# Performance work log

Hardware: AMD Instinct MI355X
Metric: run time of the kernel (lower is better)

Reference implementation:

```python
import jax, jax.numpy as jnp
import numpy as np

COMMITMENT_COST = 0.25
EPS = 1e-12  # matches torch F.normalize default eps


def _l2norm(v, axis=-1):
    n = jnp.linalg.norm(v, axis=axis, keepdims=True)
    return v / jnp.maximum(n, EPS)


def setup_inputs() -> dict:
    key = jax.random.key(0)
    k1, k2 = jax.random.split(key)
    x = jax.random.normal(k1, (65536, 256), dtype=jnp.float32)
    codebook = jax.random.normal(k2, (4096, 256), dtype=jnp.float32)
    return {"x": x, "codebook": codebook}


def reference(x, codebook):
    # x: [N, D] latents; codebook: [K, D] embedding table
    xn = _l2norm(x)                 # [N, D]
    cbn = _l2norm(codebook)         # [K, D]

    # Squared L2 distances: ||xn||^2 + ||cbn||^2 - 2 xn.cbn^T  -> [N, K]
    dists = (
        jnp.sum(xn * xn, axis=-1, keepdims=True)
        + jnp.sum(cbn * cbn, axis=1)
        - 2.0 * jnp.einsum("nd,kd->nk", xn, cbn)
    )
    idx = jnp.argmin(dists, axis=1)  # [N]

    # quantize: gather then L2-normalize (matches F.normalize(embeddings(idx)))
    quantized = _l2norm(cbn[idx])    # [N, D]

    q_latent_loss = jnp.mean((quantized - jax.lax.stop_gradient(xn)) ** 2)
    e_latent_loss = jnp.mean((xn - jax.lax.stop_gradient(quantized)) ** 2)
    loss = q_latent_loss + COMMITMENT_COST * e_latent_loss

    # straight-through estimator
    quantized_st = xn + jax.lax.stop_gradient(quantized - xn)
    return quantized_st, loss, idx
```

## Files before the change

kernel.cpp:

```cpp
#include <hip/hip_runtime.h>
#include <math.h>

#define N_ROWS 65536
#define DIM    256
#define NCODE  4096
#define MARGIN 2e-4f
#define TILE_C 32
#define NTILE  (NCODE / TILE_C)
#define FB     8
#define KCH    1024
#define NCH    (NCODE / KCH)
#define FIXG   512

typedef __attribute__((ext_vector_type(8)))  short short8v;
typedef __attribute__((ext_vector_type(4)))  float float4v;
typedef __attribute__((ext_vector_type(16))) float f32x16;

__device__ inline unsigned short f2bf(float f) {
    unsigned u = __float_as_uint(f);
    unsigned r = (u + 0x7fffu + ((u >> 16) & 1u)) >> 16;
    return (unsigned short)r;
}
__device__ inline float bf2f(unsigned short h) {
    return __uint_as_float(((unsigned)h) << 16);
}
__device__ inline void gll16(const void* g, void* l) {
    __builtin_amdgcn_global_load_lds(
        (const __attribute__((address_space(1))) unsigned int*)g,
        (__attribute__((address_space(3))) unsigned int*)l, 16, 0, 0);
}

__global__ void cb_norm_kernel(const float* __restrict__ cb,
                               unsigned short* __restrict__ pk,
                               float* __restrict__ c2,
                               double* __restrict__ c2d,
                               double* __restrict__ ndi) {
    int k = blockIdx.x;
    int t = threadIdx.x;
    float v = cb[k * DIM + t];
    double dv = (double)v;
    double ss = dv * dv;
    __shared__ double red2[4], red3[4], redn[4];
    #pragma unroll
    for (int off = 32; off > 0; off >>= 1) ss += __shfl_down(ss, off);
    if ((t & 63) == 0) redn[t >> 6] = ss;
    __syncthreads();
    double S = redn[0] + redn[1] + redn[2] + redn[3];
    double nrm = fmax(sqrt(S), 1e-12);
    double cq = dv / nrm;
    float cf = (float)cq;
    unsigned short hb = f2bf(cf);
    unsigned short lb = f2bf(cf - bf2f(hb));
    {
        int cb32 = k >> 5, klo = k & 31, ks = t >> 4, hi = (t >> 3) & 1, j = t & 7;
        size_t ch = ((size_t)cb32 * 16 + ks) * 2;
        size_t slot = (size_t)(hi * 32 + klo) * 8 + j;
        pk[(ch + 0) * 512 + slot] = hb;
        pk[(ch + 1) * 512 + slot] = lb;
    }
    double s2 = (double)cf * (double)cf;
    double s3 = cq * cq;
    #pragma unroll
    for (int off = 32; off > 0; off >>= 1) {
        s2 += __shfl_down(s2, off);
        s3 += __shfl_down(s3, off);
    }
    if ((t & 63) == 0) { red2[t >> 6] = s2; red3[t >> 6] = s3; }
    __syncthreads();
    if (t == 0) {
        c2[k]  = (float)(red2[0] + red2[1] + red2[2] + red2[3]);
        c2d[k] = red3[0] + red3[1] + red3[2] + red3[3];
        ndi[k] = 1.0 / nrm;
    }
}

__global__ void x_norm_kernel(const float* __restrict__ x,
                              float* __restrict__ nx,
                              float* __restrict__ scx,
                              int* __restrict__ counter) {
    if (blockIdx.x == 0 && threadIdx.x == 0) counter[0] = 0;
    int w = threadIdx.x >> 6;
    int lane = threadIdx.x & 63;
    int row = blockIdx.x * 4 + w;
    float4 v = ((const float4*)(x + (size_t)row * DIM))[lane];
    double ss = (double)v.x * v.x + (double)v.y * v.y
              + (double)v.z * v.z + (double)v.w * v.w;
    #pragma unroll
    for (int off = 32; off > 0; off >>= 1) ss += __shfl_down(ss, off);
    if (lane == 0) {
        double n = fmax(sqrt(ss), 1e-12);
        nx[row]  = (float)n;
        scx[row] = (float)(2.0 / n);
    }
}

__attribute__((amdgpu_waves_per_eu(2, 2)))
__global__ void __launch_bounds__(256)
argmin_mfma_kernel(const float* __restrict__ x,
                   const unsigned short* __restrict__ pk,
                   const float* __restrict__ c2,
                   const float* __restrict__ scx,
                   int* __restrict__ idx_out,
                   int* __restrict__ counter,
                   int* __restrict__ rowlist) {
    __shared__ unsigned short buf[2][16384];

    int tid  = threadIdx.x;
    int lane = tid & 63;
    int wave = tid >> 6;
    int cl31 = lane & 31;
    int hi   = lane >> 5;
    int xbase = blockIdx.x * 128 + wave * 32;

    short8v bh[16], bl[16];
    const float* xr = x + (size_t)(xbase + cl31) * DIM + hi * 8;
    #pragma unroll
    for (int ks = 0; ks < 16; ks++) {
        float4 f0 = *(const float4*)(xr + ks * 16);
        float4 f1 = *(const float4*)(xr + ks * 16 + 4);
        float e[8] = {f0.x, f0.y, f0.z, f0.w, f1.x, f1.y, f1.z, f1.w};
        short8v h, l;
        #pragma unroll
        for (int j = 0; j < 8; j++) {
            unsigned short hb = f2bf(e[j]);
            h[j] = (short)hb;
            l[j] = (short)f2bf(e[j] - bf2f(hb));
        }
        bh[ks] = h;
        bl[ks] = l;
    }
    float scr = scx[xbase + cl31];

    float s1 = 3.4e38f, s2 = 3.4e38f;
    int   i1 = 0x7fffffff;

    {
        const unsigned short* src = pk + ((size_t)wave * 8) * 512 + lane * 8;
        unsigned short* dst = &buf[0][(wave * 8) * 512];
        #pragma unroll
        for (int i = 0; i < 8; i++) gll16(src + i * 512, dst + i * 512);
    }
    __syncthreads();

    int cur = 0;
    for (int t = 0; t < NTILE; t++) {
        int cbb = t * TILE_C;

        if (t + 1 < NTILE) {
            const unsigned short* src =
                pk + ((size_t)(t + 1) * 32 + wave * 8) * 512 + lane * 8;
            unsigned short* dst = &buf[cur ^ 1][(wave * 8) * 512];
            #pragma unroll
            for (int i = 0; i < 8; i++) gll16(src + i * 512, dst + i * 512);
        }

        const unsigned short* cbuf = &buf[cur][0];
        f32x16 acc = {0.f,0.f,0.f,0.f,0.f,0.f,0.f,0.f,0.f,0.f,0.f,0.f,0.f,0.f,0.f,0.f};
        #pragma unroll
        for (int ks = 0; ks < 16; ks++) {
            short8v ah = *(const short8v*)(cbuf + (size_t)(ks * 2 + 0) * 512 + lane * 8);
            short8v al = *(const short8v*)(cbuf + (size_t)(ks * 2 + 1) * 512 + lane * 8);
            acc = __builtin_amdgcn_mfma_f32_32x32x16_bf16(ah, bh[ks], acc, 0, 0, 0);
            acc = __builtin_amdgcn_mfma_f32_32x32x16_bf16(ah, bl[ks], acc, 0, 0, 0);
            acc = __builtin_amdgcn_mfma_f32_32x32x16_bf16(al, bh[ks], acc, 0, 0, 0);
        }

        const float4v* c2p = (const float4v*)(c2 + cbb + hi * 4);
        float4v gq0 = c2p[0], gq1 = c2p[2], gq2 = c2p[4], gq3 = c2p[6];
        float sv[16];
        float mn = 3.4e38f;
        #pragma unroll
        for (int g = 0; g < 4; g++) {
            float4v gg = (g == 0) ? gq0 : (g == 1) ? gq1 : (g == 2) ? gq2 : gq3;
            #pragma unroll
            for (int q = 0; q < 4; q++) {
                float s = gg[q] - scr * acc[g * 4 + q];
                sv[g * 4 + q] = s;
                mn = fminf(mn, s);
            }
        }
        if (!__all(mn >= s2)) {
            #pragma unroll
            for (int g = 0; g < 4; g++) {
                #pragma unroll
                for (int q = 0; q < 4; q++) {
                    float s = sv[g * 4 + q];
                    int ci = cbb + q + 8 * g + 4 * hi;
                    if (s < s1) { s2 = s1; s1 = s; i1 = ci; }
                    else if (s < s2) s2 = s;
                }
            }
        }

        __syncthreads();
        cur ^= 1;
    }

    {
        float o1 = __shfl_xor(s1, 32);
        int   oi = __shfl_xor(i1, 32);
        float o2 = __shfl_xor(s2, 32);
        if (o1 < s1 || (o1 == s1 && oi < i1)) { s2 = fminf(s1, o2); s1 = o1; i1 = oi; }
        else                                   { s2 = fminf(o1, s2); }
    }
    if (lane < 32) {
        int row = xbase + lane;
        idx_out[row] = i1;
        if (s2 - s1 < MARGIN) { int slot = atomicAdd(counter, 1); rowlist[slot] = row; }
    }
}

__global__ void fixup2d_kernel(const float* __restrict__ x,
                               const float* __restrict__ cb,
                               const double* __restrict__ c2d,
                               const double* __restrict__ ndi,
                               const int* __restrict__ counter,
                               const int* __restrict__ rowlist,
                               double* __restrict__ pb_s,
                               int* __restrict__ pb_i) {
    __shared__ double xs[FB][DIM];
    __shared__ double isx_sh[FB];
    __shared__ double red_s[4][FB];
    __shared__ int    red_i[4][FB];
    int t = threadIdx.x, lane = t & 63, wave = t >> 6;
    int cnt = counter[0];
    int nbat = (cnt + FB - 1) / FB;
    int nwork = nbat * NCH;

    for (int w = blockIdx.x; w < nwork; w += FIXG) {
        int batch = w / NCH, chunk = w - batch * NCH;
        int base = batch * FB;
        int nb = cnt - base; if (nb > FB) nb = FB;

        #pragma unroll
        for (int r = 0; r < FB; r++)
            if (r < nb) xs[r][t] = (double)x[(size_t)rowlist[base + r] * DIM + t];
        __syncthreads();

        for (int rr = wave; rr < nb; rr += 4) {
            double a0 = xs[rr][lane],       a1 = xs[rr][lane + 64];
            double a2 = xs[rr][lane + 128], a3 = xs[rr][lane + 192];
            double ss = a0 * a0 + a1 * a1 + a2 * a2 + a3 * a3;
            #pragma unroll
            for (int m = 1; m < 64; m <<= 1) ss += __shfl_xor(ss, m);
            if (lane == 0) isx_sh[rr] = 2.0 / fmax(sqrt(ss), 1e-12);
        }
        __syncthreads();

        double bs[FB]; int bi[FB];
        #pragma unroll
        for (int r = 0; r < FB; r++) { bs[r] = 1e300; bi[r] = 0x7fffffff; }

        for (int k0 = 0; k0 < KCH / 256; k0++) {
            int k = chunk * KCH + k0 * 256 + t;
            const float4* cr = (const float4*)(cb + (size_t)k * DIM);
            double d[FB];
            #pragma unroll
            for (int r = 0; r < FB; r++) d[r] = 0.0;
            #pragma unroll 4
            for (int d4 = 0; d4 < DIM / 4; d4++) {
                float4 c = cr[d4];
                double cx = c.x, cy = c.y, cz = c.z, cw = c.w;
                int dd = d4 * 4;
                #pragma unroll
                for (int r = 0; r < FB; r++) {
                    d[r] = fma(cx, xs[r][dd],     d[r]);
                    d[r] = fma(cy, xs[r][dd + 1], d[r]);
                    d[r] = fma(cz, xs[r][dd + 2], d[r]);
                    d[r] = fma(cw, xs[r][dd + 3], d[r]);
                }
            }
            double ndik = ndi[k], c2k = c2d[k];
            #pragma unroll
            for (int r = 0; r < FB; r++) {
                double sc = c2k - isx_sh[r] * d[r] * ndik;
                if (sc < bs[r] || (sc == bs[r] && k < bi[r])) { bs[r] = sc; bi[r] = k; }
            }
        }

        #pragma unroll
        for (int r = 0; r < FB; r++) {
            double b = bs[r]; int idx = bi[r];
            #pragma unroll
            for (int m = 1; m < 64; m <<= 1) {
                double ob = __shfl_xor(b, m);
                int   oi = __shfl_xor(idx, m);
                if (ob < b || (ob == b && oi < idx)) { b = ob; idx = oi; }
            }
            if (lane == 0) { red_s[wave][r] = b; red_i[wave][r] = idx; }
        }
        __syncthreads();
        if (t < nb) {
            double b = red_s[0][t]; int idx = red_i[0][t];
            #pragma unroll
            for (int ww = 1; ww < 4; ww++) {
                double ob = red_s[ww][t]; int oi = red_i[ww][t];
                if (ob < b || (ob == b && oi < idx)) { b = ob; idx = oi; }
            }
            pb_s[(size_t)(base + t) * NCH + chunk] = b;
            pb_i[(size_t)(base + t) * NCH + chunk] = idx;
        }
        __syncthreads();
    }
}

__global__ void fixmerge_kernel(const int* __restrict__ counter,
                                const int* __restrict__ rowlist,
                                const double* __restrict__ pb_s,
                                const int* __restrict__ pb_i,
                                int* __restrict__ idxv) {
    int cnt = counter[0];
    for (int s = blockIdx.x * 256 + threadIdx.x; s < cnt; s += gridDim.x * 256) {
        double b = pb_s[(size_t)s * NCH]; int idx = pb_i[(size_t)s * NCH];
        #pragma unroll
        for (int c = 1; c < NCH; c++) {
            double ob = pb_s[(size_t)s * NCH + c]; int oi = pb_i[(size_t)s * NCH + c];
            if (ob < b || (ob == b && oi < idx)) { b = ob; idx = oi; }
        }
        idxv[rowlist[s]] = idx;
    }
}

__global__ void gather_loss_kernel(const float* __restrict__ x,
                                   const float* __restrict__ cb,
                                   const double* __restrict__ ndi,
                                   const float* __restrict__ nx,
                                   const int* __restrict__ idxv,
                                   float* __restrict__ out_q,
                                   float* __restrict__ out_idxf,
                                   float* __restrict__ partials) {
    int w = threadIdx.x >> 6, lane = threadIdx.x & 63;
    int row = blockIdx.x * 4 + w;
    int iv = idxv[row];
    float ndif = (float)ndi[iv];
    float inx = 1.0f / nx[row];
    float4 q4 = ((const float4*)(cb + (size_t)iv * DIM))[lane];
    float4 x4 = ((const float4*)(x + (size_t)row * DIM))[lane];
    float4 qq;
    qq.x = q4.x * ndif; qq.y = q4.y * ndif;
    qq.z = q4.z * ndif; qq.w = q4.w * ndif;
    ((float4*)(out_q + (size_t)row * DIM))[lane] = qq;
    float dx = qq.x - x4.x * inx;
    float dy = qq.y - x4.y * inx;
    float dz = qq.z - x4.z * inx;
    float dw = qq.w - x4.w * inx;
    float ss = dx * dx + dy * dy + dz * dz + dw * dw;
    #pragma unroll
    for (int off = 32; off > 0; off >>= 1) ss += __shfl_down(ss, off);
    if (lane == 0) {
        partials[row] = ss;
        out_idxf[row] = (float)iv;
    }
}

__global__ void loss_reduce_kernel(const float* __restrict__ partials,
                                   float* __restrict__ out_loss) {
    int t = threadIdx.x;
    float s = 0.0f;
    for (int i = t; i < N_ROWS; i += 256) s += partials[i];
    __shared__ float red[4];
    #pragma unroll
    for (int off = 32; off > 0; off >>= 1) s += __shfl_down(s, off);
    if ((t & 63) == 0) red[t >> 6] = s;
    __syncthreads();
    if (t == 0) out_loss[0] = 1.25f * (red[0] + red[1] + red[2] + red[3]) / (float)(N_ROWS * DIM);
}

extern "C" void kernel_launch(void* const* d_in, const int* in_sizes, int n_in,
                              void* d_out, int out_size, void* d_ws, size_t ws_size,
                              hipStream_t stream) {
    const float* x  = (const float*)d_in[0];
    const float* cb = (const float*)d_in[1];
    float* out = (float*)d_out;

    double* c2d  = (double*)d_ws;
    double* ndi  = c2d + NCODE;
    double* pb_s = ndi + NCODE;
    float*  c2   = (float*)(pb_s + (size_t)N_ROWS * NCH);
    float*  nx   = c2 + NCODE;
    float*  scx  = nx + N_ROWS;
    int*    idxv = (int*)(scx + N_ROWS);
    float*  partials = (float*)(idxv + N_ROWS);
    int*    counter  = (int*)(partials + N_ROWS);
    int*    rowlist  = counter + 8;
    int*    pb_i     = rowlist + N_ROWS;
    unsigned short* pk = (unsigned short*)(pb_i + (size_t)N_ROWS * NCH);

    float* out_q    = out;
    float* out_loss = out + (size_t)N_ROWS * DIM;
    float* out_idxf = out_loss + 1;

    hipLaunchKernelGGL(cb_norm_kernel, dim3(NCODE), dim3(256), 0, stream,
                       cb, pk, c2, c2d, ndi);
    hipLaunchKernelGGL(x_norm_kernel, dim3(N_ROWS / 4), dim3(256), 0, stream, x, nx, scx, counter);
    hipLaunchKernelGGL(argmin_mfma_kernel, dim3(N_ROWS / 128), dim3(256), 0, stream,
                       x, pk, c2, scx, idxv, counter, rowlist);
    hipLaunchKernelGGL(fixup2d_kernel, dim3(FIXG), dim3(256), 0, stream,
                       x, cb, c2d, ndi, counter, rowlist, pb_s, pb_i);
    hipLaunchKernelGGL(fixmerge_kernel, dim3(64), dim3(256), 0, stream,
                       counter, rowlist, pb_s, pb_i, idxv);
    hipLaunchKernelGGL(gather_loss_kernel, dim3(N_ROWS / 4), dim3(256), 0, stream,
                       x, cb, ndi, nx, idxv, out_q, out_idxf, partials);
    hipLaunchKernelGGL(loss_reduce_kernel, dim3(1), dim3(256), 0, stream,
                       partials, out_loss);
}
```

Measured before the change: 599.3 us.

## Halve LDS codebook buffer with half-tile pipelining to double occupancy

The two-slot LDS double buffer of 32 KB per tile is replaced by a single 32 KB buffer split into two K-halves. Each loop phase prefetches the next half while computing MFMAs on the current one, and the argmin update runs only after the second half. The waves-per-EU hint is raised from 2 to 4, so more blocks fit per CU and can hide latency. The cost is twice as many __syncthreads barriers and more register pressure under the tighter occupancy target, because the bh/bl split-bf16 fragments still have to stay in registers.

```diff
diff --git a/kernel.cpp b/kernel.cpp
--- a/kernel.cpp
+++ b/kernel.cpp
@@ -94,7 +94,7 @@
     }
 }
 
-__attribute__((amdgpu_waves_per_eu(2, 2)))
+__attribute__((amdgpu_waves_per_eu(4, 4)))
 __global__ void __launch_bounds__(256)
 argmin_mfma_kernel(const float* __restrict__ x,
                    const unsigned short* __restrict__ pk,
@@ -103,7 +103,7 @@
                    int* __restrict__ idx_out,
                    int* __restrict__ counter,
                    int* __restrict__ rowlist) {
-    __shared__ unsigned short buf[2][16384];
+    __shared__ unsigned short buf[16384];
 
     int tid  = threadIdx.x;
     int lane = tid & 63;
@@ -135,65 +135,72 @@
     int   i1 = 0x7fffffff;
 
     {
-        const unsigned short* src = pk + ((size_t)wave * 8) * 512 + lane * 8;
-        unsigned short* dst = &buf[0][(wave * 8) * 512];
-        #pragma unroll
-        for (int i = 0; i < 8; i++) gll16(src + i * 512, dst + i * 512);
+        const unsigned short* src = pk + ((size_t)(wave * 4)) * 512 + lane * 8;
+        unsigned short* dst = &buf[(wave * 4) * 512];
+        #pragma unroll
+        for (int i = 0; i < 4; i++) gll16(src + i * 512, dst + i * 512);
     }
     __syncthreads();
 
-    int cur = 0;
-    for (int t = 0; t < NTILE; t++) {
-        int cbb = t * TILE_C;
-
-        if (t + 1 < NTILE) {
+    f32x16 acc = {0.f,0.f,0.f,0.f,0.f,0.f,0.f,0.f,0.f,0.f,0.f,0.f,0.f,0.f,0.f,0.f};
+    for (int ph = 0; ph < 2 * NTILE; ph++) {
+        int t = ph >> 1;
+        int h = ph & 1;
+
+        int st = h ? t + 1 : t;
+        int sh = h ^ 1;
+        if (st < NTILE) {
             const unsigned short* src =
-                pk + ((size_t)(t + 1) * 32 + wave * 8) * 512 + lane * 8;
-            unsigned short* dst = &buf[cur ^ 1][(wave * 8) * 512];
-            #pragma unroll
-            for (int i = 0; i < 8; i++) gll16(src + i * 512, dst + i * 512);
-        }
-
-        const unsigned short* cbuf = &buf[cur][0];
-        f32x16 acc = {0.f,0.f,0.f,0.f,0.f,0.f,0.f,0.f,0.f,0.f,0.f,0.f,0.f,0.f,0.f,0.f};
-        #pragma unroll
-        for (int ks = 0; ks < 16; ks++) {
+                pk + ((size_t)st * 32 + sh * 16 + wave * 4) * 512 + lane * 8;
+            unsigned short* dst = &buf[(sh * 16 + wave * 4) * 512];
+            #pragma unroll
+            for (int i = 0; i < 4; i++) gll16(src + i * 512, dst + i * 512);
+        }
+
+        const unsigned short* cbuf = &buf[(h * 16) * 512];
+        #pragma unroll
+        for (int ks = 0; ks < 8; ks++) {
             short8v ah = *(const short8v*)(cbuf + (size_t)(ks * 2 + 0) * 512 + lane * 8);
             short8v al = *(const short8v*)(cbuf + (size_t)(ks * 2 + 1) * 512 + lane * 8);
-            acc = __builtin_amdgcn_mfma_f32_32x32x16_bf16(ah, bh[ks], acc, 0, 0, 0);
-            acc = __builtin_amdgcn_mfma_f32_32x32x16_bf16(ah, bl[ks], acc, 0, 0, 0);
-            acc = __builtin_amdgcn_mfma_f32_32x32x16_bf16(al, bh[ks], acc, 0, 0, 0);
-        }
-
-        const float4v* c2p = (const float4v*)(c2 + cbb + hi * 4);
-        float4v gq0 = c2p[0], gq1 = c2p[2], gq2 = c2p[4], gq3 = c2p[6];
-        float sv[16];
-        float mn = 3.4e38f;
-        #pragma unroll
-        for (int g = 0; g < 4; g++) {
-            float4v gg = (g == 0) ? gq0 : (g == 1) ? gq1 : (g == 2) ? gq2 : gq3;
-            #pragma unroll
-            for (int q = 0; q < 4; q++) {
-                float s = gg[q] - scr * acc[g * 4 + q];
-                sv[g * 4 + q] = s;
-                mn = fminf(mn, s);
-            }
-        }
-        if (!__all(mn >= s2)) {
+            int kg = h * 8 + ks;
+            acc = __builtin_amdgcn_mfma_f32_32x32x16_bf16(ah, bh[kg], acc, 0, 0, 0);
+            acc = __builtin_amdgcn_mfma_f32_32x32x16_bf16(ah, bl[kg], acc, 0, 0, 0);
+            acc = __builtin_amdgcn_mfma_f32_32x32x16_bf16(al, bh[kg], acc, 0, 0, 0);
+        }
+
+        if (h == 1) {
+            int cbb = t * TILE_C;
+            const float4v* c2p = (const float4v*)(c2 + cbb + hi * 4);
+            float4v gq0 = c2p[0], gq1 = c2p[2], gq2 = c2p[4], gq3 = c2p[6];
+            float sv[16];
+            float mn = 3.4e38f;
             #pragma unroll
             for (int g = 0; g < 4; g++) {
+                float4v gg = (g == 0) ? gq0 : (g == 1) ? gq1 : (g == 2) ? gq2 : gq3;
                 #pragma unroll
                 for (int q = 0; q < 4; q++) {
-                    float s = sv[g * 4 + q];
-                    int ci = cbb + q + 8 * g + 4 * hi;
-                    if (s < s1) { s2 = s1; s1 = s; i1 = ci; }
-                    else if (s < s2) s2 = s;
+                    float s = gg[q] - scr * acc[g * 4 + q];
+                    sv[g * 4 + q] = s;
+                    mn = fminf(mn, s);
                 }
             }
+            if (!__all(mn >= s2)) {
+                #pragma unroll
+                for (int g = 0; g < 4; g++) {
+                    #pragma unroll
+                    for (int q = 0; q < 4; q++) {
+                        float s = sv[g * 4 + q];
+                        int ci = cbb + q + 8 * g + 4 * hi;
+                        if (s < s1) { s2 = s1; s1 = s; i1 = ci; }
+                        else if (s < s2) s2 = s;
+                    }
+                }
+            }
+            #pragma unroll
+            for (int r = 0; r < 16; r++) acc[r] = 0.f;
         }
 
         __syncthreads();
-        cur ^= 1;
     }
 
     {
```

After: 1.437 ms. 2.4x slower.
